# Kernel tuning notes

Measured on AMD Instinct MI355X. Metric: run time of the kernel, lower is better.

## Reference

```python
import jax, jax.numpy as jnp
import numpy as np

HEADS = 16
LN_EPS = 1e-5


def setup_inputs() -> dict:
    key = jax.random.key(0)
    ks = jax.random.split(key, 4)
    B, S, C, U = 2, 2048, 1024, 1024
    scale = 1.0 / np.sqrt(C)
    return {
        "inputs": jax.random.normal(ks[0], (B, S, C), dtype=jnp.float32),
        "Wq": jax.random.normal(ks[1], (C, U), dtype=jnp.float32) * scale,
        "bq": jnp.zeros((U,), dtype=jnp.float32),
        "Wk": jax.random.normal(ks[2], (C, U), dtype=jnp.float32) * scale,
        "bk": jnp.zeros((U,), dtype=jnp.float32),
        "Wv": jax.random.normal(ks[3], (C, U), dtype=jnp.float32) * scale,
        "bv": jnp.zeros((U,), dtype=jnp.float32),
        "ln_gamma": jnp.ones((S, U), dtype=jnp.float32),
        "ln_beta": jnp.zeros((S, U), dtype=jnp.float32),
    }


def reference(inputs, Wq, bq, Wk, bk, Wv, bv, ln_gamma, ln_beta):
    B, S, C = inputs.shape
    U = Wq.shape[1]
    H = HEADS
    dh = U // H

    Q = inputs @ Wq + bq  # [B,S,U]
    K = inputs @ Wk + bk
    V = inputs @ Wv + bv

    # torch: concat(split(X, U//H, dim=-1), dim=0) -> head-major stacking on batch
    def split_heads(X):
        return jnp.moveaxis(X.reshape(B, S, H, dh), 2, 0).reshape(H * B, S, dh)

    Q_, K_, V_ = split_heads(Q), split_heads(K), split_heads(V)

    scores = jnp.einsum('bqd,bkd->bqk', Q_, K_) / jnp.sqrt(jnp.float32(dh))
    tri = jnp.tril(jnp.ones((S, S), dtype=bool))  # causal mask
    scores = jnp.where(tri[None, :, :], scores, jnp.float32(-1e9))
    attn = jax.nn.softmax(scores, axis=-1)
    out_ = jnp.einsum('bqk,bkd->bqd', attn, V_)  # [H*B,S,dh]

    # inverse: split on batch into H chunks of size B, concat on feature dim
    out = jnp.moveaxis(out_.reshape(H, B, S, dh), 0, 2).reshape(B, S, U)

    out = out + inputs  # residual

    # LayerNorm over normalized_shape=[S, U] (joint seq+feature stats)
    mu = jnp.mean(out, axis=(-2, -1), keepdims=True)
    var = jnp.mean(jnp.square(out - mu), axis=(-2, -1), keepdims=True)
    out = (out - mu) / jnp.sqrt(var + LN_EPS) * ln_gamma + ln_beta
    return out
```

## Files before the change

### kernel.cpp

```cpp
#include <hip/hip_runtime.h>
#include <hip/hip_bf16.h>


typedef __bf16 bf16_t;
typedef __bf16 bf16x8 __attribute__((ext_vector_type(8)));
typedef __bf16 bf16x4 __attribute__((ext_vector_type(4)));
typedef _Float16 f16_t;
typedef _Float16 f16x4 __attribute__((ext_vector_type(4)));
typedef _Float16 f16x8 __attribute__((ext_vector_type(8)));
typedef float f32x4 __attribute__((ext_vector_type(4)));

constexpr int Bsz = 2;
constexpr int Seq = 2048;
constexpr int Cdim = 1024;
constexpr int Udim = 1024;
constexpr int Hn = 16;
constexpr int Dh = 64;
constexpr int Mrows = Bsz * Seq;
constexpr int PerBatch = Seq * Udim;
constexpr float SCLQ = 0.125f * 1.44269504088896340736f;
constexpr float M0 = 10.0f;

__device__ __forceinline__ void gload16(const void* g, void* l)
{
    __builtin_amdgcn_global_load_lds(
        (const __attribute__((address_space(1))) void*)g,
        (__attribute__((address_space(3))) void*)l, 16, 0, 0);
}

__global__ __launch_bounds__(256)
void cast_x(const float* __restrict__ X, bf16_t* __restrict__ Xb)
{
    int i = blockIdx.x * 256 + threadIdx.x;
    float4 v = ((const float4*)X)[i];
    bf16x4 o = { (bf16_t)v.x, (bf16_t)v.y, (bf16_t)v.z, (bf16_t)v.w };
    *(bf16x4*)(Xb + (size_t)i * 4) = o;
}

__global__ void transpose_w(const float* __restrict__ Wq, const float* __restrict__ Wk,
                            const float* __restrict__ Wv,
                            bf16_t* __restrict__ Tq, bf16_t* __restrict__ Tk,
                            bf16_t* __restrict__ Tv)
{
    int z = blockIdx.z;
    const float* W = (z == 0) ? Wq : (z == 1) ? Wk : Wv;
    bf16_t* T = (z == 0) ? Tq : (z == 1) ? Tk : Tv;
    __shared__ bf16_t t[64][65];
    int x0 = blockIdx.x * 64, y0 = blockIdx.y * 64;
    int tx = threadIdx.x;
    for (int i = threadIdx.y; i < 64; i += 8)
        t[i][tx] = (bf16_t)W[(size_t)(y0 + i) * Cdim + x0 + tx];
    __syncthreads();
    for (int i = threadIdx.y; i < 64; i += 8)
        T[(size_t)(x0 + i) * Cdim + y0 + tx] = t[tx][i];
}

__global__ __launch_bounds__(256)
void gemm_qkv(const bf16_t* __restrict__ X,
              const bf16_t* __restrict__ Wt0, const bf16_t* __restrict__ Wt1,
              const bf16_t* __restrict__ Wt2,
              const float* __restrict__ b0, const float* __restrict__ b1,
              const float* __restrict__ b2,
              f16_t* __restrict__ O0, f16_t* __restrict__ O1, f16_t* __restrict__ O2)
{
    int z = blockIdx.z;
    const bf16_t* Wt = (z == 0) ? Wt0 : (z == 1) ? Wt1 : Wt2;
    const float* bias = (z == 0) ? b0 : (z == 1) ? b1 : b2;
    f16_t* Og = (z == 0) ? O0 : (z == 1) ? O1 : O2;
    float scl = (z == 0) ? SCLQ : 1.0f;

    constexpr int Kd = 1024, Nd = 1024;
    __shared__ __align__(16) bf16_t As[128 * 32];
    __shared__ __align__(16) bf16_t Bs[128 * 32];

    int tid = threadIdx.x;
    int wave = tid >> 6, lane = tid & 63, quad = lane >> 4, l16 = lane & 15;
    int wm = (wave & 1) * 64, wn = (wave >> 1) * 64;
    int m0 = blockIdx.y * 128, n0 = blockIdx.x * 128;

    f32x4 acc[4][4] = {};

    int e0 = wave * 512 + lane * 8;
    int r0 = e0 >> 5, c0 = e0 & 31;
    int e1 = e0 + 2048;
    int r1 = e1 >> 5, c1 = e1 & 31;
    const bf16_t* Ag = X + (size_t)m0 * Kd;
    const bf16_t* Bg = Wt + (size_t)n0 * Kd;
    bf16_t* AsW0 = As + wave * 512;
    bf16_t* AsW1 = As + 2048 + wave * 512;
    bf16_t* BsW0 = Bs + wave * 512;
    bf16_t* BsW1 = Bs + 2048 + wave * 512;

    for (int k0 = 0; k0 < Kd; k0 += 32) {
        gload16(Ag + (size_t)r0 * Kd + k0 + c0, AsW0);
        gload16(Ag + (size_t)r1 * Kd + k0 + c1, AsW1);
        gload16(Bg + (size_t)r0 * Kd + k0 + c0, BsW0);
        gload16(Bg + (size_t)r1 * Kd + k0 + c1, BsW1);
        __syncthreads();

        bf16x8 af[4], bfr[4];
#pragma unroll
        for (int i = 0; i < 4; i++)
            af[i] = *(const bf16x8*)&As[(wm + i * 16 + l16) * 32 + quad * 8];
#pragma unroll
        for (int i = 0; i < 4; i++)
            bfr[i] = *(const bf16x8*)&Bs[(wn + i * 16 + l16) * 32 + quad * 8];
#pragma unroll
        for (int mt = 0; mt < 4; mt++)
#pragma unroll
            for (int nt = 0; nt < 4; nt++)
                acc[mt][nt] = __builtin_amdgcn_mfma_f32_16x16x32_bf16(
                    af[mt], bfr[nt], acc[mt][nt], 0, 0, 0);
        __syncthreads();
    }

#pragma unroll
    for (int nt = 0; nt < 4; nt++) {
        int col = n0 + wn + nt * 16 + l16;
        float bv = bias[col];
#pragma unroll
        for (int mt = 0; mt < 4; mt++) {
            int row = m0 + wm + mt * 16 + quad * 4;
#pragma unroll
            for (int r = 0; r < 4; r++)
                Og[(size_t)(row + r) * Nd + col] = (f16_t)((acc[mt][nt][r] + bv) * scl);
        }
    }
}

__global__ void transpose_v(const f16_t* __restrict__ V, f16_t* __restrict__ Vt)
{
    int s0 = blockIdx.x * 64;
    int y = blockIdx.y;
    int b = y >> 4, h = y & 15;
    __shared__ f16_t t[64][65];
    int tx = threadIdx.x;
    for (int i = threadIdx.y; i < 64; i += 8)
        t[i][tx] = V[(size_t)(b * Seq + s0 + i) * Udim + h * Dh + tx];
    __syncthreads();
    for (int i = threadIdx.y; i < 64; i += 8)
        Vt[((size_t)y * Dh + i) * Seq + s0 + tx] = t[tx][i];
}

__global__ __launch_bounds__(256)
void attn6(const f16_t* __restrict__ Q, const f16_t* __restrict__ K,
           const f16_t* __restrict__ Vt, const float* __restrict__ X,
           float* __restrict__ R, float* __restrict__ stats)
{
    int id = blockIdx.x;
    int c = id & 7;
    int r8 = id >> 3;
    int g = r8 & 3;
    int kk = r8 >> 2;
    int bh = (g << 3) | c;
    int b = bh >> 4, h = bh & 15;
    int qtile = 31 - kk;

    int tid = threadIdx.x;
    int w = tid >> 6, lane = tid & 63, quad = lane >> 4, l16 = lane & 15;
    size_t bS = (size_t)b * Seq;

    __shared__ f16_t Ks[2][64][72];
    __shared__ f16_t Vs[2][64][72];

    const f16_t* Kg = K + bS * Udim + h * Dh;
    const f16_t* Vg = Vt + ((size_t)(b * Hn + h)) * Dh * Seq;

    int sr = tid >> 2, sc = (tid & 3) * 16;
    int q0 = qtile * 64 + w * 16;
    int qidx = q0 + l16;

    const f16_t* Qp = Q + (bS + qidx) * Udim + h * Dh;
    f16x8 qf[2];
#pragma unroll
    for (int s = 0; s < 2; s++) qf[s] = *(const f16x8*)(Qp + s * 32 + quad * 8);

    f32x4 Oacc[4] = {};
    float lsum = 0.0f;

    {
        const f16_t* kp = Kg + (size_t)sr * Udim + sc;
        const f16_t* vp = Vg + (size_t)sr * Seq + sc;
        f16x8 k0 = *(const f16x8*)kp;
        f16x8 k1 = *(const f16x8*)(kp + 8);
        f16x8 v0 = *(const f16x8*)vp;
        f16x8 v1 = *(const f16x8*)(vp + 8);
        *(f16x8*)&Ks[0][sr][sc] = k0;
        *(f16x8*)&Ks[0][sr][sc + 8] = k1;
        *(f16x8*)&Vs[0][sr][sc] = v0;
        *(f16x8*)&Vs[0][sr][sc + 8] = v1;
    }
    __syncthreads();

    int buf = 0;
    for (int i = 0; i < qtile; i++) {
        int kvn = i * 64 + 64;
        const f16_t* kp = Kg + (size_t)(kvn + sr) * Udim + sc;
        const f16_t* vp = Vg + (size_t)sr * Seq + kvn + sc;
        f16x8 nk0 = *(const f16x8*)kp;
        f16x8 nk1 = *(const f16x8*)(kp + 8);
        f16x8 nv0 = *(const f16x8*)vp;
        f16x8 nv1 = *(const f16x8*)(vp + 8);

        f32x4 st[4];
#pragma unroll
        for (int t = 0; t < 4; t++) {
            f32x4 a = {};
#pragma unroll
            for (int s = 0; s < 2; s++) {
                f16x8 kf = *(const f16x8*)&Ks[buf][t * 16 + l16][s * 32 + quad * 8];
                a = __builtin_amdgcn_mfma_f32_16x16x32_f16(kf, qf[s], a, 0, 0, 0);
            }
            st[t] = a;
        }

        f16x4 pf[4];
#pragma unroll
        for (int t = 0; t < 4; t++)
#pragma unroll
            for (int r = 0; r < 4; r++) {
                float pv = exp2f(st[t][r] - M0);
                lsum += pv;
                pf[t][r] = (f16_t)pv;
            }

#pragma unroll
        for (int t = 0; t < 4; t++)
#pragma unroll
            for (int dt = 0; dt < 4; dt++) {
                f16x4 vf = *(const f16x4*)&Vs[buf][dt * 16 + l16][t * 16 + quad * 4];
                Oacc[dt] = __builtin_amdgcn_mfma_f32_16x16x16f16(vf, pf[t], Oacc[dt], 0, 0, 0);
            }

        *(f16x8*)&Ks[buf ^ 1][sr][sc] = nk0;
        *(f16x8*)&Ks[buf ^ 1][sr][sc + 8] = nk1;
        *(f16x8*)&Vs[buf ^ 1][sr][sc] = nv0;
        *(f16x8*)&Vs[buf ^ 1][sr][sc + 8] = nv1;
        __syncthreads();
        buf ^= 1;
    }

    {
        int kv0 = qtile * 64;
#pragma unroll
        for (int t = 0; t < 4; t++) {
            if (t <= w) {
                f32x4 a = {};
#pragma unroll
                for (int s = 0; s < 2; s++) {
                    f16x8 kf = *(const f16x8*)&Ks[buf][t * 16 + l16][s * 32 + quad * 8];
                    a = __builtin_amdgcn_mfma_f32_16x16x32_f16(kf, qf[s], a, 0, 0, 0);
                }
                f16x4 pfd;
#pragma unroll
                for (int r = 0; r < 4; r++) {
                    float sv = a[r];
                    if (kv0 + t * 16 + quad * 4 + r > qidx) sv = -1e30f;
                    float pv = exp2f(sv - M0);
                    lsum += pv;
                    pfd[r] = (f16_t)pv;
                }
#pragma unroll
                for (int dt = 0; dt < 4; dt++) {
                    f16x4 vf = *(const f16x4*)&Vs[buf][dt * 16 + l16][t * 16 + quad * 4];
                    Oacc[dt] = __builtin_amdgcn_mfma_f32_16x16x16f16(vf, pfd, Oacc[dt], 0, 0, 0);
                }
            }
        }
    }

    lsum += __shfl_xor(lsum, 16);
    lsum += __shfl_xor(lsum, 32);
    float invl = 1.0f / lsum;

    float s_acc = 0.0f, ss_acc = 0.0f;
    const float* Xp = X + (bS + qidx) * Udim + h * Dh;
    float* Rp = R + (bS + qidx) * Udim + h * Dh;
#pragma unroll
    for (int dt = 0; dt < 4; dt++) {
        f32x4 xv = *(const f32x4*)(Xp + dt * 16 + quad * 4);
        f32x4 o = Oacc[dt] * invl + xv;
        *(f32x4*)(Rp + dt * 16 + quad * 4) = o;
#pragma unroll
        for (int r = 0; r < 4; r++) {
            s_acc += o[r];
            ss_acc += o[r] * o[r];
        }
    }

#pragma unroll
    for (int o = 1; o < 64; o <<= 1) {
        s_acc += __shfl_xor(s_acc, o);
        ss_acc += __shfl_xor(ss_acc, o);
    }
    __shared__ float red[8];
    if (lane == 0) { red[w] = s_acc; red[4 + w] = ss_acc; }
    __syncthreads();
    if (tid == 0) {
        atomicAdd(&stats[b], red[0] + red[1] + red[2] + red[3]);
        atomicAdd(&stats[2 + b], red[4] + red[5] + red[6] + red[7]);
    }
}

__global__ __launch_bounds__(256)
void ln_norm(const float* __restrict__ R, const float* __restrict__ gamma,
             const float* __restrict__ beta, const float* __restrict__ stats,
             float* __restrict__ out)
{
    constexpr int TOT4 = Bsz * Seq * Udim / 4;
    constexpr float invN = 1.0f / (float)PerBatch;
    float mu[2], inv[2];
    for (int b = 0; b < 2; b++) {
        float m = stats[b] * invN;
        float var = stats[2 + b] * invN - m * m;
        mu[b] = m;
        inv[b] = rsqrtf(var + 1e-5f);
    }
    for (int i = blockIdx.x * blockDim.x + threadIdx.x; i < TOT4;
         i += gridDim.x * blockDim.x) {
        int f = i * 4;
        int b = f >> 21;
        int su = f & (PerBatch - 1);
        float4 rv = *(const float4*)(R + f);
        float4 g = *(const float4*)(gamma + su);
        float4 be = *(const float4*)(beta + su);
        float4 o;
        o.x = (rv.x - mu[b]) * inv[b] * g.x + be.x;
        o.y = (rv.y - mu[b]) * inv[b] * g.y + be.y;
        o.z = (rv.z - mu[b]) * inv[b] * g.z + be.z;
        o.w = (rv.w - mu[b]) * inv[b] * g.w + be.w;
        *(float4*)(out + f) = o;
    }
}

extern "C" void kernel_launch(void* const* d_in, const int* in_sizes, int n_in,
                              void* d_out, int out_size, void* d_ws, size_t ws_size,
                              hipStream_t stream)
{
    const float* X     = (const float*)d_in[0];
    const float* Wq    = (const float*)d_in[1];
    const float* bq    = (const float*)d_in[2];
    const float* Wk    = (const float*)d_in[3];
    const float* bk    = (const float*)d_in[4];
    const float* Wv    = (const float*)d_in[5];
    const float* bv    = (const float*)d_in[6];
    const float* gamma = (const float*)d_in[7];
    const float* beta  = (const float*)d_in[8];
    float* out = (float*)d_out;

    char* ws = (char*)d_ws;
    size_t off = 0;
    auto alloc = [&](size_t bytes) -> void* {
        void* p = ws + off;
        off += (bytes + 255) & ~(size_t)255;
        return p;
    };
    bf16_t* Xb = (bf16_t*)alloc((size_t)Mrows * Cdim * 2);
    bf16_t* Tq = (bf16_t*)alloc((size_t)Cdim * Udim * 2);
    bf16_t* Tk = (bf16_t*)alloc((size_t)Cdim * Udim * 2);
    bf16_t* Tv = (bf16_t*)alloc((size_t)Cdim * Udim * 2);
    f16_t*  Qb = (f16_t*)alloc((size_t)Mrows * Udim * 2);
    f16_t*  Kb = (f16_t*)alloc((size_t)Mrows * Udim * 2);
    f16_t*  Vb = (f16_t*)alloc((size_t)Mrows * Udim * 2);
    f16_t*  Vtb = (f16_t*)alloc((size_t)Mrows * Udim * 2);
    float*  Rb = (float*)alloc((size_t)Mrows * Udim * 4);
    float*  stats = (float*)alloc(4 * sizeof(float));

    hipMemsetAsync(stats, 0, 4 * sizeof(float), stream);
    cast_x<<<dim3(Mrows * Cdim / 4 / 256), 256, 0, stream>>>(X, Xb);
    transpose_w<<<dim3(16, 16, 3), dim3(64, 8), 0, stream>>>(Wq, Wk, Wv, Tq, Tk, Tv);
    gemm_qkv<<<dim3(8, 32, 3), 256, 0, stream>>>(Xb, Tq, Tk, Tv, bq, bk, bv, Qb, Kb, Vb);
    transpose_v<<<dim3(Seq / 64, Bsz * Hn), dim3(64, 8), 0, stream>>>(Vb, Vtb);
    attn6<<<dim3(1024), 256, 0, stream>>>(Qb, Kb, Vtb, X, Rb, stats);
    ln_norm<<<dim3(1024), 256, 0, stream>>>(Rb, gamma, beta, stats, out);
}
```

Measured before the change: 198.5 us.

## Fuse prep kernels and write V transposed directly from QKV GEMM epilogue

Merges the X cast, weight transposes and the stats zeroing into one prep launch, which removes the memset and a separate kernel. The QKV GEMM now writes V straight into the per-head transposed layout with packed 4-element stores, so the transpose_v kernel and its extra V round-trip through memory go away. The cost is strided stores from the GEMM epilogue for V. The prep blocks are also less uniform in their work.

```diff
diff --git a/kernel.cpp b/kernel.cpp
--- a/kernel.cpp
+++ b/kernel.cpp
@@ -29,30 +29,38 @@
 }
 
 __global__ __launch_bounds__(256)
-void cast_x(const float* __restrict__ X, bf16_t* __restrict__ Xb)
-{
-    int i = blockIdx.x * 256 + threadIdx.x;
-    float4 v = ((const float4*)X)[i];
-    bf16x4 o = { (bf16_t)v.x, (bf16_t)v.y, (bf16_t)v.z, (bf16_t)v.w };
-    *(bf16x4*)(Xb + (size_t)i * 4) = o;
-}
-
-__global__ void transpose_w(const float* __restrict__ Wq, const float* __restrict__ Wk,
-                            const float* __restrict__ Wv,
-                            bf16_t* __restrict__ Tq, bf16_t* __restrict__ Tk,
-                            bf16_t* __restrict__ Tv)
+void prep(const float* __restrict__ X,
+          const float* __restrict__ Wq, const float* __restrict__ Wk,
+          const float* __restrict__ Wv,
+          bf16_t* __restrict__ Xb,
+          bf16_t* __restrict__ Tq, bf16_t* __restrict__ Tk,
+          bf16_t* __restrict__ Tv, float* __restrict__ stats)
 {
     int z = blockIdx.z;
-    const float* W = (z == 0) ? Wq : (z == 1) ? Wk : Wv;
-    bf16_t* T = (z == 0) ? Tq : (z == 1) ? Tk : Tv;
-    __shared__ bf16_t t[64][65];
-    int x0 = blockIdx.x * 64, y0 = blockIdx.y * 64;
-    int tx = threadIdx.x;
-    for (int i = threadIdx.y; i < 64; i += 8)
-        t[i][tx] = (bf16_t)W[(size_t)(y0 + i) * Cdim + x0 + tx];
-    __syncthreads();
-    for (int i = threadIdx.y; i < 64; i += 8)
-        T[(size_t)(x0 + i) * Cdim + y0 + tx] = t[tx][i];
+    int tid = threadIdx.x;
+    if (z < 3) {
+        const float* W = (z == 0) ? Wq : (z == 1) ? Wk : Wv;
+        bf16_t* T = (z == 0) ? Tq : (z == 1) ? Tk : Tv;
+        __shared__ bf16_t t[64][65];
+        int x0 = blockIdx.x * 64, y0 = blockIdx.y * 64;
+        int tx = tid & 63, ty = tid >> 6;
+        for (int i = ty; i < 64; i += 4)
+            t[i][tx] = (bf16_t)W[(size_t)(y0 + i) * Cdim + x0 + tx];
+        __syncthreads();
+        for (int i = ty; i < 64; i += 4)
+            T[(size_t)(x0 + i) * Cdim + y0 + tx] = t[tx][i];
+    } else {
+        int bi = blockIdx.y * 16 + blockIdx.x;
+        if (bi == 0 && tid < 4) stats[tid] = 0.0f;
+        const float4* Xv = (const float4*)X;
+#pragma unroll
+        for (int k = 0; k < 16; k++) {
+            int i = bi * 4096 + k * 256 + tid;
+            float4 v = Xv[i];
+            bf16x4 o = { (bf16_t)v.x, (bf16_t)v.y, (bf16_t)v.z, (bf16_t)v.w };
+            *(bf16x4*)(Xb + (size_t)i * 4) = o;
+        }
+    }
 }
 
 __global__ __launch_bounds__(256)
@@ -61,12 +69,11 @@
               const bf16_t* __restrict__ Wt2,
               const float* __restrict__ b0, const float* __restrict__ b1,
               const float* __restrict__ b2,
-              f16_t* __restrict__ O0, f16_t* __restrict__ O1, f16_t* __restrict__ O2)
+              f16_t* __restrict__ O0, f16_t* __restrict__ O1, f16_t* __restrict__ O2v)
 {
     int z = blockIdx.z;
     const bf16_t* Wt = (z == 0) ? Wt0 : (z == 1) ? Wt1 : Wt2;
     const float* bias = (z == 0) ? b0 : (z == 1) ? b1 : b2;
-    f16_t* Og = (z == 0) ? O0 : (z == 1) ? O1 : O2;
     float scl = (z == 0) ? SCLQ : 1.0f;
 
     constexpr int Kd = 1024, Nd = 1024;
@@ -114,32 +121,39 @@
         __syncthreads();
     }
 
-#pragma unroll
-    for (int nt = 0; nt < 4; nt++) {
-        int col = n0 + wn + nt * 16 + l16;
-        float bv = bias[col];
-#pragma unroll
-        for (int mt = 0; mt < 4; mt++) {
-            int row = m0 + wm + mt * 16 + quad * 4;
-#pragma unroll
-            for (int r = 0; r < 4; r++)
-                Og[(size_t)(row + r) * Nd + col] = (f16_t)((acc[mt][nt][r] + bv) * scl);
-        }
-    }
-}
-
-__global__ void transpose_v(const f16_t* __restrict__ V, f16_t* __restrict__ Vt)
-{
-    int s0 = blockIdx.x * 64;
-    int y = blockIdx.y;
-    int b = y >> 4, h = y & 15;
-    __shared__ f16_t t[64][65];
-    int tx = threadIdx.x;
-    for (int i = threadIdx.y; i < 64; i += 8)
-        t[i][tx] = V[(size_t)(b * Seq + s0 + i) * Udim + h * Dh + tx];
-    __syncthreads();
-    for (int i = threadIdx.y; i < 64; i += 8)
-        Vt[((size_t)y * Dh + i) * Seq + s0 + tx] = t[tx][i];
+    if (z < 2) {
+        f16_t* Og = (z == 0) ? O0 : O1;
+#pragma unroll
+        for (int nt = 0; nt < 4; nt++) {
+            int col = n0 + wn + nt * 16 + l16;
+            float bv = bias[col];
+#pragma unroll
+            for (int mt = 0; mt < 4; mt++) {
+                int row = m0 + wm + mt * 16 + quad * 4;
+#pragma unroll
+                for (int r = 0; r < 4; r++)
+                    Og[(size_t)(row + r) * Nd + col] = (f16_t)((acc[mt][nt][r] + bv) * scl);
+            }
+        }
+    } else {
+        int bb = m0 >> 11;
+#pragma unroll
+        for (int nt = 0; nt < 4; nt++) {
+            int col = n0 + wn + nt * 16 + l16;
+            float bv = bias[col];
+            int h = col >> 6, d = col & 63;
+            f16_t* vbase = O2v + (((size_t)(bb * Hn + h) * Dh + d) << 11);
+#pragma unroll
+            for (int mt = 0; mt < 4; mt++) {
+                int row = m0 + wm + mt * 16 + quad * 4;
+                int s = row & (Seq - 1);
+                f16x4 pk;
+#pragma unroll
+                for (int r = 0; r < 4; r++) pk[r] = (f16_t)(acc[mt][nt][r] + bv);
+                *(f16x4*)(vbase + s) = pk;
+            }
+        }
+    }
 }
 
 __global__ __launch_bounds__(256)
@@ -361,16 +375,12 @@
     bf16_t* Tv = (bf16_t*)alloc((size_t)Cdim * Udim * 2);
     f16_t*  Qb = (f16_t*)alloc((size_t)Mrows * Udim * 2);
     f16_t*  Kb = (f16_t*)alloc((size_t)Mrows * Udim * 2);
-    f16_t*  Vb = (f16_t*)alloc((size_t)Mrows * Udim * 2);
     f16_t*  Vtb = (f16_t*)alloc((size_t)Mrows * Udim * 2);
     float*  Rb = (float*)alloc((size_t)Mrows * Udim * 4);
     float*  stats = (float*)alloc(4 * sizeof(float));
 
-    hipMemsetAsync(stats, 0, 4 * sizeof(float), stream);
-    cast_x<<<dim3(Mrows * Cdim / 4 / 256), 256, 0, stream>>>(X, Xb);
-    transpose_w<<<dim3(16, 16, 3), dim3(64, 8), 0, stream>>>(Wq, Wk, Wv, Tq, Tk, Tv);
-    gemm_qkv<<<dim3(8, 32, 3), 256, 0, stream>>>(Xb, Tq, Tk, Tv, bq, bk, bv, Qb, Kb, Vb);
-    transpose_v<<<dim3(Seq / 64, Bsz * Hn), dim3(64, 8), 0, stream>>>(Vb, Vtb);
+    prep<<<dim3(16, 16, 4), 256, 0, stream>>>(X, Wq, Wk, Wv, Xb, Tq, Tk, Tv, stats);
+    gemm_qkv<<<dim3(8, 32, 3), 256, 0, stream>>>(Xb, Tq, Tk, Tv, bq, bk, bv, Qb, Kb, Vtb);
     attn6<<<dim3(1024), 256, 0, stream>>>(Qb, Kb, Vtb, X, Rb, stats);
     ln_norm<<<dim3(1024), 256, 0, stream>>>(Rb, gamma, beta, stats, out);
 }
```

Result: faster. 193.7 us (-2.4%).
